# Kernel optimization log

Measured on AMD Instinct MI355X. Metric: run time of the kernel, lower is better.

The kernel has to match this reference:

```python
import jax, jax.numpy as jnp
import numpy as np

B, C, L = 8, 256, 4096
OC = C // 2  # out_channels default
EPS = 1e-5


def setup_inputs() -> dict:
    key = jax.random.key(0)
    ks = jax.random.split(key, 12)
    s_in = 1.0 / np.sqrt(C)   # conv1d default init scale (kaiming-uniform-ish)
    s_oc = 1.0 / np.sqrt(OC)
    return {
        "x": jax.random.normal(ks[0], (B, C, L), dtype=jnp.float32),
        "g_w": jax.random.uniform(ks[1], (OC, C), jnp.float32, -s_in, s_in),
        "g_b": jax.random.uniform(ks[2], (OC,), jnp.float32, -s_in, s_in),
        # theta/phi weights: nn.init.normal_(w, 0.02) -> mean 0.02, std 1
        "theta_w": 0.02 + jax.random.normal(ks[3], (OC, C), dtype=jnp.float32),
        "theta_b": jax.random.uniform(ks[4], (OC,), jnp.float32, -s_in, s_in),
        "phi_w": 0.02 + jax.random.normal(ks[5], (OC, C), dtype=jnp.float32),
        "phi_b": jax.random.uniform(ks[6], (OC,), jnp.float32, -s_in, s_in),
        "W_w": jax.random.uniform(ks[7], (C, OC), jnp.float32, -s_oc, s_oc),
        "W_b": jax.random.uniform(ks[8], (C,), jnp.float32, -s_oc, s_oc),
        # BN affine: init to zero in the original; use small random for a meaningful test
        "gamma": 0.1 * jax.random.normal(ks[9], (C,), dtype=jnp.float32),
        "beta": 0.1 * jax.random.normal(ks[10], (C,), dtype=jnp.float32),
    }


def reference(x, g_w, g_b, theta_w, theta_b, phi_w, phi_b, W_w, W_b, gamma, beta):
    # x: (b, c, l). 1x1 conv == per-position linear map over channels.
    g_x = jnp.einsum('oc,bcl->bol', g_w, x) + g_b[None, :, None]        # (b, oc, l)
    theta_x = jnp.einsum('oc,bcl->bol', theta_w, x) + theta_b[None, :, None]
    phi_x = jnp.einsum('oc,bcl->bol', phi_w, x) + phi_b[None, :, None]
    # f = theta^T phi : (b, l, l) quadratic score matrix (no softmax)
    f = jnp.einsum('bok,bom->bkm', theta_x, phi_x)
    N = f.shape[-1]
    # y = (f @ g^T) / N, returned in (b, oc, l) layout
    y = jnp.einsum('bkm,bom->bok', f, g_x) / N
    W_y = jnp.einsum('co,bol->bcl', W_w, y) + W_b[None, :, None]        # (b, c, l)
    # BatchNorm1d (training mode: batch statistics over (b, l), biased var)
    mean = jnp.mean(W_y, axis=(0, 2), keepdims=True)
    var = jnp.mean((W_y - mean) ** 2, axis=(0, 2), keepdims=True)
    W_y = (W_y - mean) * jax.lax.rsqrt(var + EPS)
    W_y = gamma[None, :, None] * W_y + beta[None, :, None]
    return W_y + x  # residual
```

## Files before the change

kernel.cpp:

```cpp
#include <hip/hip_runtime.h>
#include <hip/hip_bf16.h>

#define B_ 8
#define C_ 256
#define OC_ 128
#define L_ 4096
#define EPS_ 1e-5f
#define SPLITK 8

typedef unsigned short u16;
typedef __attribute__((ext_vector_type(4))) unsigned short u16x4;
typedef __attribute__((ext_vector_type(4))) float f32x4;
typedef __attribute__((ext_vector_type(8))) short bf16x8;

__device__ inline u16 f2bf(float f) {
  union { __hip_bfloat16 h; u16 u; } v;
  v.h = __float2bfloat16(f);
  return v.u;
}
__device__ inline float bf2f(u16 u) {
  union { float f; unsigned u; } v;
  v.u = ((unsigned)u) << 16;
  return v.f;
}

__device__ inline void gload_lds16(const void* g, void* lds) {
  __builtin_amdgcn_global_load_lds(
      (const __attribute__((address_space(1))) unsigned int*)g,
      (__attribute__((address_space(3))) unsigned int*)lds, 16, 0, 0);
}

__global__ __launch_bounds__(256) void k_cvt(const float* __restrict__ x,
                                             u16* __restrict__ Xb,
                                             u16* __restrict__ XbT,
                                             float* __restrict__ spartial) {
  __shared__ u16 T[64][73];
  __shared__ float P[64][17];
  const int b = blockIdx.z, c0 = blockIdx.y * 64, l0 = blockIdx.x * 64;
  const int tid = threadIdx.x;
#pragma unroll
  for (int it = 0; it < 4; ++it) {
    int idx = it * 256 + tid;
    int row = idx >> 4;
    int col = (idx & 15) << 2;
    size_t gi = ((size_t)(b * C_ + c0 + row)) * L_ + l0 + col;
    float4 v = *(const float4*)(x + gi);
    u16 u0 = f2bf(v.x), u1 = f2bf(v.y), u2 = f2bf(v.z), u3 = f2bf(v.w);
    u16x4 u = {u0, u1, u2, u3};
    *(u16x4*)(Xb + gi) = u;
    T[row][col] = u0; T[row][col + 1] = u1; T[row][col + 2] = u2; T[row][col + 3] = u3;
    P[row][idx & 15] = v.x + v.y + v.z + v.w;
  }
  __syncthreads();
  if (tid < 64) {
    float acc = 0.f;
#pragma unroll
    for (int j = 0; j < 16; j++) acc += P[tid][j];
    spartial[(size_t)blockIdx.x * (B_ * C_) + b * C_ + c0 + tid] = acc;
  }
#pragma unroll
  for (int it = 0; it < 4; ++it) {
    int idx = it * 256 + tid;
    int lrow = idx >> 4;
    int ccol = (idx & 15) << 2;
    u16x4 u = {T[ccol][lrow], T[ccol + 1][lrow], T[ccol + 2][lrow], T[ccol + 3][lrow]};
    *(u16x4*)(XbT + ((size_t)b * L_ + l0 + lrow) * C_ + c0 + ccol) = u;
  }
}

__global__ __launch_bounds__(256) void k_xxt(const u16* __restrict__ Xb,
                                             float* __restrict__ Spart) {
  const int b = blockIdx.z, split = blockIdx.y;
  const int ti = blockIdx.x >> 2, tj = blockIdx.x & 3;
  __shared__ u16 lds[2][2][64 * 64];
  const int tid = threadIdx.x, lane = tid & 63;
  const int wid = tid >> 6, wr = wid >> 1, wc = wid & 1;
  const u16* Arows = Xb + ((size_t)b * C_ + ti * 64) * L_;
  const u16* Brows = Xb + ((size_t)b * C_ + tj * 64) * L_;
  const int k0 = split * (L_ / SPLITK);
  f32x4 acc[2][2] = {};

  auto STAGE = [&](int buf, int kt) {
#pragma unroll
    for (int ch = 0; ch < 2; ch++) {
      int d = ch * 4096 + tid * 16;
      int row = d >> 7;
      int kb = (d & 127) ^ ((row & 7) << 4);
      gload_lds16(Arows + (size_t)row * L_ + k0 + kt + (kb >> 1), (char*)lds[buf][0] + d);
      gload_lds16(Brows + (size_t)row * L_ + k0 + kt + (kb >> 1), (char*)lds[buf][1] + d);
    }
  };

  STAGE(0, 0);
  asm volatile("s_waitcnt vmcnt(0)" ::: "memory");
  __syncthreads();
  int cur = 0;
  for (int kt = 0; kt < L_ / SPLITK; kt += 64) {
    if (kt + 64 < L_ / SPLITK) STAGE(cur ^ 1, kt + 64);
#pragma unroll
    for (int kk = 0; kk < 2; kk++) {
      bf16x8 af[2], bfr[2];
#pragma unroll
      for (int m = 0; m < 2; m++) {
        int row = wr * 32 + m * 16 + (lane & 15);
        int kb = ((kk << 6) + ((lane >> 4) << 4)) ^ ((row & 7) << 4);
        af[m] = *(const bf16x8*)((const char*)lds[cur][0] + row * 128 + kb);
      }
#pragma unroll
      for (int n = 0; n < 2; n++) {
        int row = wc * 32 + n * 16 + (lane & 15);
        int kb = ((kk << 6) + ((lane >> 4) << 4)) ^ ((row & 7) << 4);
        bfr[n] = *(const bf16x8*)((const char*)lds[cur][1] + row * 128 + kb);
      }
#pragma unroll
      for (int m = 0; m < 2; m++)
#pragma unroll
        for (int n = 0; n < 2; n++)
          acc[m][n] = __builtin_amdgcn_mfma_f32_16x16x32_bf16(af[m], bfr[n], acc[m][n], 0, 0, 0);
    }
    asm volatile("s_waitcnt vmcnt(0)" ::: "memory");
    __syncthreads();
    cur ^= 1;
  }
  float* Sp = Spart + ((size_t)split * B_ + b) * C_ * C_;
#pragma unroll
  for (int m = 0; m < 2; m++)
#pragma unroll
    for (int n = 0; n < 2; n++) {
      int r0 = ti * 64 + wr * 32 + m * 16 + ((lane >> 4) << 2);
      int c0 = tj * 64 + wc * 32 + n * 16 + (lane & 15);
#pragma unroll
      for (int r = 0; r < 4; r++)
        Sp[(size_t)(r0 + r) * C_ + c0] = acc[m][n][r];
    }
}

__global__ __launch_bounds__(256) void k_sreduce(const float* __restrict__ Spart,
                                                 const float* __restrict__ spartial,
                                                 const float* __restrict__ g_w,
                                                 float* __restrict__ S,
                                                 u16* __restrict__ Sb,
                                                 float* __restrict__ s,
                                                 float* __restrict__ gwT) {
  const int bid = blockIdx.x, tid = threadIdx.x;
  if (bid < (B_ * C_ * C_) / 256) {
    size_t idx = (size_t)bid * 256 + tid;
    float acc = 0.f;
    for (int sp = 0; sp < SPLITK; sp++) acc += Spart[(size_t)sp * B_ * C_ * C_ + idx];
    S[idx] = acc;
    Sb[idx] = f2bf(acc);
  } else if (bid < (B_ * C_ * C_) / 256 + (B_ * C_) / 256) {
    int idx2 = (bid - (B_ * C_ * C_) / 256) * 256 + tid;
    float acc = 0.f;
#pragma unroll 8
    for (int i = 0; i < 64; i++) acc += spartial[(size_t)i * (B_ * C_) + idx2];
    s[idx2] = acc;
  } else {
    int t = bid - ((B_ * C_ * C_) / 256 + (B_ * C_) / 256);
    int o = t * 8 + (tid & 7);
    int cbase = (tid >> 3) * 8;
#pragma unroll
    for (int k = 0; k < 8; k++) {
      int c = cbase + k;
      gwT[c * OC_ + o] = g_w[o * C_ + c];
    }
  }
}

__global__ __launch_bounds__(256) void k_mid1(const float* __restrict__ S,
                                              const float* __restrict__ s,
                                              const float* __restrict__ phi_w,
                                              const float* __restrict__ phi_b,
                                              const float* __restrict__ gwT,
                                              const float* __restrict__ g_b,
                                              float* __restrict__ MT) {
  const int b = blockIdx.x >> 5, ot = blockIdx.x & 31;
  const int tid = threadIdx.x;
  __shared__ float pw[4][257], t2[4][257], sl[256], ps_s[4], pb_s[4], redw[4][4];
  sl[tid] = s[b * C_ + tid];
#pragma unroll
  for (int r = 0; r < 4; r++) pw[r][tid] = phi_w[(ot * 4 + r) * C_ + tid];
  if (tid < 4) pb_s[tid] = phi_b[ot * 4 + tid];
  __syncthreads();
  float acc4[4] = {};
  const float* Sbr = S + (size_t)b * C_ * C_;
#pragma unroll 4
  for (int cp = 0; cp < C_; cp++) {
    float sv = Sbr[(size_t)cp * C_ + tid];
#pragma unroll
    for (int r = 0; r < 4; r++) acc4[r] += pw[r][cp] * sv;
  }
  const int lane = tid & 63, w = tid >> 6;
#pragma unroll
  for (int r = 0; r < 4; r++) {
    float v = pw[r][tid] * sl[tid];
#pragma unroll
    for (int off = 1; off < 64; off <<= 1) v += __shfl_xor(v, off, 64);
    if (lane == 0) redw[w][r] = v;
  }
#pragma unroll
  for (int r = 0; r < 4; r++) t2[r][tid] = acc4[r] + pb_s[r] * sl[tid];
  __syncthreads();
  if (tid < 4) ps_s[tid] = redw[0][tid] + redw[1][tid] + redw[2][tid] + redw[3][tid];
  __syncthreads();
  const int o = tid & 127, half = tid >> 7;
  float m0 = 0.f, m1 = 0.f;
#pragma unroll 4
  for (int c = 0; c < C_; c++) {
    float gv = gwT[c * OC_ + o];
    m0 += t2[half * 2][c] * gv;
    m1 += t2[half * 2 + 1][c] * gv;
  }
  float gb = g_b[o];
  int r0 = half * 2;
  MT[((size_t)b * OC_ + o) * OC_ + ot * 4 + r0]     = m0 + (ps_s[r0] + (float)L_ * pb_s[r0]) * gb;
  MT[((size_t)b * OC_ + o) * OC_ + ot * 4 + r0 + 1] = m1 + (ps_s[r0 + 1] + (float)L_ * pb_s[r0 + 1]) * gb;
}

__global__ __launch_bounds__(256) void k_mid2(const float* __restrict__ MT,
                                              const float* __restrict__ W_w,
                                              const float* __restrict__ theta_w,
                                              const float* __restrict__ theta_b,
                                              const float* __restrict__ W_b,
                                              const float* __restrict__ s,
                                              u16* __restrict__ Qb,
                                              float* __restrict__ qv,
                                              float* __restrict__ qs_g,
                                              float* __restrict__ sum1) {
  const int b = blockIdx.x >> 6, ct = blockIdx.x & 63;
  const int c0 = ct * 4;
  const int tid = threadIdx.x;
  __shared__ float ww[4][OC_], u_s[4][OC_ + 2], s_l[C_], q_s[4], redq[4][4];
  s_l[tid] = s[b * C_ + tid];
#pragma unroll
  for (int i = tid; i < 4 * OC_; i += 256)
    ww[i >> 7][i & 127] = W_w[(c0 + (i >> 7)) * OC_ + (i & 127)];
  __syncthreads();
  const int op = tid & 127, rh = tid >> 7;
  float ua0 = 0.f, ua1 = 0.f;
  const float* MTb = MT + (size_t)b * OC_ * OC_;
#pragma unroll 4
  for (int o = 0; o < OC_; o++) {
    float mv = MTb[(size_t)o * OC_ + op];
    ua0 += ww[rh * 2][o] * mv;
    ua1 += ww[rh * 2 + 1][o] * mv;
  }
  u_s[rh * 2][op] = ua0 * (1.f / (float)L_);
  u_s[rh * 2 + 1][op] = ua1 * (1.f / (float)L_);
  __syncthreads();
  {
    const int r = tid >> 6, lane = tid & 63;
    float v = u_s[r][lane] * theta_b[lane] + u_s[r][lane + 64] * theta_b[lane + 64];
#pragma unroll
    for (int off = 1; off < 64; off <<= 1) v += __shfl_xor(v, off, 64);
    if (lane == 0) {
      float qval = v + W_b[c0 + r];
      q_s[r] = qval;
      qv[b * C_ + c0 + r] = qval;
    }
  }
  float qa[4] = {};
#pragma unroll 2
  for (int o = 0; o < OC_; o++) {
    float tv = theta_w[(size_t)o * C_ + tid];
#pragma unroll
    for (int r = 0; r < 4; r++) qa[r] += u_s[r][o] * tv;
  }
#pragma unroll
  for (int r = 0; r < 4; r++)
    Qb[((size_t)b * C_ + c0 + r) * C_ + tid] = f2bf(qa[r]);
  const int lane = tid & 63, w = tid >> 6;
#pragma unroll
  for (int r = 0; r < 4; r++) {
    float v = qa[r] * s_l[tid];
#pragma unroll
    for (int off = 1; off < 64; off <<= 1) v += __shfl_xor(v, off, 64);
    if (lane == 0) redq[w][r] = v;
  }
  __syncthreads();
  if (tid < 4) {
    float qs = redq[0][tid] + redq[1][tid] + redq[2][tid] + redq[3][tid];
    qs_g[b * C_ + c0 + tid] = qs;
    sum1[b * C_ + c0 + tid] = qs + (float)L_ * q_s[tid];
  }
}

__global__ __launch_bounds__(256) void k_ystat(const u16* __restrict__ Qb,
                                               const u16* __restrict__ Sb,
                                               float* __restrict__ e2part) {
  const int b = blockIdx.z;
  const int chs = blockIdx.y >> 1, ct = blockIdx.y & 1;
  const int ks = blockIdx.x;
  __shared__ u16 lds[2 * 128 * 64];
  __shared__ float e2s[128][2];
  const int tid = threadIdx.x, lane = tid & 63;
  const int wid = tid >> 6, wr = wid >> 1, wc = wid & 1;
  const u16* Abase = Qb + ((size_t)b * C_ + ct * 128) * C_;
  const u16* Bbase = Sb + ((size_t)b * C_ + chs * 128) * C_;
  const int k0 = ks * 64;
  f32x4 acc[4][4] = {};
#pragma unroll
  for (int ch = 0; ch < 4; ch++) {
    int d = ch * 4096 + tid * 16;
    int row = d >> 7;
    int kb = (d & 127) ^ ((row & 7) << 4);
    gload_lds16(Abase + (size_t)row * C_ + k0 + (kb >> 1), (char*)lds + d);
    gload_lds16(Bbase + (size_t)row * C_ + k0 + (kb >> 1), (char*)lds + 16384 + d);
  }
  asm volatile("s_waitcnt vmcnt(0)" ::: "memory");
  __syncthreads();
#pragma unroll
  for (int kk = 0; kk < 2; kk++) {
    bf16x8 af[4], bfr[4];
#pragma unroll
    for (int m = 0; m < 4; m++) {
      int row = wr * 64 + m * 16 + (lane & 15);
      int kb = ((kk << 6) + ((lane >> 4) << 4)) ^ ((row & 7) << 4);
      af[m] = *(const bf16x8*)((const char*)lds + row * 128 + kb);
    }
#pragma unroll
    for (int n = 0; n < 4; n++) {
      int row = wc * 64 + n * 16 + (lane & 15);
      int kb = ((kk << 6) + ((lane >> 4) << 4)) ^ ((row & 7) << 4);
      bfr[n] = *(const bf16x8*)((const char*)lds + 16384 + row * 128 + kb);
    }
#pragma unroll
    for (int m = 0; m < 4; m++)
#pragma unroll
      for (int n = 0; n < 4; n++)
        acc[m][n] = __builtin_amdgcn_mfma_f32_16x16x32_bf16(af[m], bfr[n], acc[m][n], 0, 0, 0);
  }
  float e2a[4][4];
#pragma unroll
  for (int m = 0; m < 4; m++)
#pragma unroll
    for (int r = 0; r < 4; r++) e2a[m][r] = 0.f;
#pragma unroll
  for (int m = 0; m < 4; m++)
#pragma unroll
    for (int n = 0; n < 4; n++) {
      int ch = chs * 128 + wc * 64 + n * 16 + (lane & 15);
#pragma unroll
      for (int r = 0; r < 4; r++) {
        int c_loc = wr * 64 + m * 16 + ((lane >> 4) << 2) + r;
        float q2 = bf2f(Qb[((size_t)b * C_ + ct * 128 + c_loc) * C_ + ch]);
        e2a[m][r] += acc[m][n][r] * q2;
      }
    }
#pragma unroll
  for (int m = 0; m < 4; m++)
#pragma unroll
    for (int r = 0; r < 4; r++) {
      float v = e2a[m][r];
      v += __shfl_xor(v, 1, 64);
      v += __shfl_xor(v, 2, 64);
      v += __shfl_xor(v, 4, 64);
      v += __shfl_xor(v, 8, 64);
      if ((lane & 15) == 0) {
        int c_loc = wr * 64 + m * 16 + ((lane >> 4) << 2) + r;
        e2s[c_loc][wc] = v;
      }
    }
  __syncthreads();
  if (tid < 128)
    e2part[(((size_t)chs * 4 + ks) * B_ + b) * C_ + ct * 128 + tid] =
        e2s[tid][0] + e2s[tid][1];
}

__global__ __launch_bounds__(256) void k_fin(const float* __restrict__ sum1,
                                             const float* __restrict__ e2part,
                                             const float* __restrict__ qv,
                                             const float* __restrict__ qs_g,
                                             const float* __restrict__ gamma,
                                             const float* __restrict__ beta,
                                             float* __restrict__ gsc_g,
                                             float* __restrict__ qp_g) {
  const int b = blockIdx.x, c = threadIdx.x;
  float m = 0.f, e = 0.f;
#pragma unroll
  for (int bb = 0; bb < B_; bb++) {
    m += sum1[bb * C_ + c];
    float e2 = 0.f;
#pragma unroll
    for (int sl = 0; sl < 8; sl++) e2 += e2part[((size_t)sl * B_ + bb) * C_ + c];
    float qq = qv[bb * C_ + c], qs = qs_g[bb * C_ + c];
    e += e2 + 2.f * qq * qs + (float)L_ * qq * qq;
  }
  const float inv_n = 1.f / (float)(B_ * L_);
  m *= inv_n;
  e *= inv_n;
  float var = e - m * m;
  float g = gamma[c] * rsqrtf(var + EPS_);
  if (b == 0) gsc_g[c] = g;
  qp_g[b * C_ + c] = g * (qv[b * C_ + c] - m) + beta[c];
}

__global__ __launch_bounds__(256) void k_out(const u16* __restrict__ Qb,
                                             const float* __restrict__ gsc_g,
                                             const float* __restrict__ qp_g,
                                             const u16* __restrict__ XbT,
                                             const u16* __restrict__ Xb,
                                             float* __restrict__ out) {
  const int b = blockIdx.z, ct = blockIdx.y, lt = blockIdx.x;
  __shared__ u16 lds[2][2 * 128 * 64];
  __shared__ float gsc_s[128], qp_s[128];
  const int tid = threadIdx.x, lane = tid & 63;
  const int wid = tid >> 6, wr = wid >> 1, wc = wid & 1;
  if (tid < 128) {
    gsc_s[tid] = gsc_g[ct * 128 + tid];
    qp_s[tid] = qp_g[b * C_ + ct * 128 + tid];
  }
  const u16* Abase = Qb + ((size_t)b * C_ + ct * 128) * C_;
  const u16* Bbase = XbT + ((size_t)b * L_ + lt * 128) * C_;
  f32x4 acc[4][4] = {};
  auto STAGE = [&](int buf, int k0) {
#pragma unroll
    for (int ch = 0; ch < 4; ch++) {
      int d = ch * 4096 + tid * 16;
      int row = d >> 7;
      int kb = (d & 127) ^ ((row & 7) << 4);
      gload_lds16(Abase + (size_t)row * C_ + k0 + (kb >> 1), (char*)lds[buf] + d);
      gload_lds16(Bbase + (size_t)row * C_ + k0 + (kb >> 1), (char*)lds[buf] + 16384 + d);
    }
  };
  STAGE(0, 0);
  asm volatile("s_waitcnt vmcnt(0)" ::: "memory");
  __syncthreads();
  int cur = 0;
  for (int k0 = 0; k0 < C_; k0 += 64) {
    if (k0 + 64 < C_) STAGE(cur ^ 1, k0 + 64);
#pragma unroll
    for (int kk = 0; kk < 2; kk++) {
      bf16x8 af[4], bfr[4];
#pragma unroll
      for (int m = 0; m < 4; m++) {
        int row = wr * 64 + m * 16 + (lane & 15);
        int kb = ((kk << 6) + ((lane >> 4) << 4)) ^ ((row & 7) << 4);
        af[m] = *(const bf16x8*)((const char*)lds[cur] + row * 128 + kb);
      }
#pragma unroll
      for (int n = 0; n < 4; n++) {
        int row = wc * 64 + n * 16 + (lane & 15);
        int kb = ((kk << 6) + ((lane >> 4) << 4)) ^ ((row & 7) << 4);
        bfr[n] = *(const bf16x8*)((const char*)lds[cur] + 16384 + row * 128 + kb);
      }
#pragma unroll
      for (int m = 0; m < 4; m++)
#pragma unroll
        for (int n = 0; n < 4; n++)
          acc[m][n] = __builtin_amdgcn_mfma_f32_16x16x32_bf16(af[m], bfr[n], acc[m][n], 0, 0, 0);
    }
    asm volatile("s_waitcnt vmcnt(0)" ::: "memory");
    __syncthreads();
    cur ^= 1;
  }
#pragma unroll
  for (int m = 0; m < 4; m++)
#pragma unroll
    for (int n = 0; n < 4; n++) {
      int cl = wr * 64 + m * 16 + ((lane >> 4) << 2);
      int c = ct * 128 + cl;
      int l = lt * 128 + wc * 64 + n * 16 + (lane & 15);
#pragma unroll
      for (int r = 0; r < 4; r++) {
        size_t gi = ((size_t)b * C_ + c + r) * L_ + l;
        out[gi] = gsc_s[cl + r] * acc[m][n][r] + bf2f(Xb[gi]) + qp_s[cl + r];
      }
    }
}

extern "C" void kernel_launch(void* const* d_in, const int* in_sizes, int n_in,
                              void* d_out, int out_size, void* d_ws, size_t ws_size,
                              hipStream_t stream) {
  const float* x       = (const float*)d_in[0];
  const float* g_w     = (const float*)d_in[1];
  const float* g_b     = (const float*)d_in[2];
  const float* theta_w = (const float*)d_in[3];
  const float* theta_b = (const float*)d_in[4];
  const float* phi_w   = (const float*)d_in[5];
  const float* phi_b   = (const float*)d_in[6];
  const float* W_w     = (const float*)d_in[7];
  const float* W_b     = (const float*)d_in[8];
  const float* gamma   = (const float*)d_in[9];
  const float* beta    = (const float*)d_in[10];
  float* out = (float*)d_out;

  float* ws = (float*)d_ws;
  size_t off = 0;
  float* Spart    = ws + off; off += (size_t)SPLITK * B_ * C_ * C_;
  float* S        = ws + off; off += (size_t)B_ * C_ * C_;
  float* spartial = ws + off; off += (size_t)B_ * C_ * 64;
  float* s_       = ws + off; off += B_ * C_;
  float* gwT      = ws + off; off += C_ * OC_;
  float* MT       = ws + off; off += (size_t)B_ * OC_ * OC_;
  float* qv       = ws + off; off += B_ * C_;
  float* qs_g     = ws + off; off += B_ * C_;
  float* sum1     = ws + off; off += B_ * C_;
  float* e2part   = ws + off; off += 8 * B_ * C_;
  float* gsc_g    = ws + off; off += C_;
  float* qp_g     = ws + off; off += B_ * C_;
  u16* Sb  = (u16*)(ws + off); off += (size_t)B_ * C_ * C_ / 2;
  u16* Qb  = (u16*)(ws + off); off += (size_t)B_ * C_ * C_ / 2;
  u16* Xb  = (u16*)(ws + off); off += (size_t)B_ * C_ * L_ / 2;
  u16* XbT = (u16*)(ws + off); off += (size_t)B_ * C_ * L_ / 2;

  k_cvt<<<dim3(L_ / 64, C_ / 64, B_), 256, 0, stream>>>(x, Xb, XbT, spartial);
  k_xxt<<<dim3(16, SPLITK, B_), 256, 0, stream>>>(Xb, Spart);
  k_sreduce<<<(B_ * C_ * C_) / 256 + (B_ * C_) / 256 + 16, 256, 0, stream>>>(
      Spart, spartial, g_w, S, Sb, s_, gwT);
  k_mid1<<<B_ * 32, 256, 0, stream>>>(S, s_, phi_w, phi_b, gwT, g_b, MT);
  k_mid2<<<B_ * 64, 256, 0, stream>>>(MT, W_w, theta_w, theta_b, W_b, s_,
                                      Qb, qv, qs_g, sum1);
  k_ystat<<<dim3(4, 4, B_), 256, 0, stream>>>(Qb, Sb, e2part);
  k_fin<<<B_, 256, 0, stream>>>(sum1, e2part, qv, qs_g, gamma, beta, gsc_g, qp_g);
  k_out<<<dim3(L_ / 128, C_ / 128, B_), 256, 0, stream>>>(
      Qb, gsc_g, qp_g, XbT, Xb, out);
}
```

Before: 126.7 us.

## Fold BN scale and residual identity into Q matrix; drop LDS staging in output GEMM

The BN finalize step moves into a new k_build kernel, which scales each row of Q by the BN gain and adds the identity matrix. The residual x is then produced inside the output GEMM from XbT, so the extra read of Xb in the epilogue goes away. k_out now loads MFMA fragments straight from global memory without LDS double-buffering. The k_cvt transpose tile layout also changes. A side effect is that the residual now goes through bf16 rounding after being summed with the scaled Q, which may cost some accuracy.

```diff
diff --git a/kernel.cpp b/kernel.cpp
--- a/kernel.cpp
+++ b/kernel.cpp
@@ -10,6 +10,7 @@
 
 typedef unsigned short u16;
 typedef __attribute__((ext_vector_type(4))) unsigned short u16x4;
+typedef __attribute__((ext_vector_type(8))) unsigned short u16x8;
 typedef __attribute__((ext_vector_type(4))) float f32x4;
 typedef __attribute__((ext_vector_type(8))) short bf16x8;
 
@@ -34,7 +35,7 @@
                                              u16* __restrict__ Xb,
                                              u16* __restrict__ XbT,
                                              float* __restrict__ spartial) {
-  __shared__ u16 T[64][73];
+  __shared__ u16 T[64 * 65];
   __shared__ float P[64][17];
   const int b = blockIdx.z, c0 = blockIdx.y * 64, l0 = blockIdx.x * 64;
   const int tid = threadIdx.x;
@@ -48,7 +49,10 @@
     u16 u0 = f2bf(v.x), u1 = f2bf(v.y), u2 = f2bf(v.z), u3 = f2bf(v.w);
     u16x4 u = {u0, u1, u2, u3};
     *(u16x4*)(Xb + gi) = u;
-    T[row][col] = u0; T[row][col + 1] = u1; T[row][col + 2] = u2; T[row][col + 3] = u3;
+    T[(col + 0) * 65 + row] = u0;
+    T[(col + 1) * 65 + row] = u1;
+    T[(col + 2) * 65 + row] = u2;
+    T[(col + 3) * 65 + row] = u3;
     P[row][idx & 15] = v.x + v.y + v.z + v.w;
   }
   __syncthreads();
@@ -63,7 +67,8 @@
     int idx = it * 256 + tid;
     int lrow = idx >> 4;
     int ccol = (idx & 15) << 2;
-    u16x4 u = {T[ccol][lrow], T[ccol + 1][lrow], T[ccol + 2][lrow], T[ccol + 3][lrow]};
+    u16x4 u = {T[lrow * 65 + ccol], T[lrow * 65 + ccol + 1],
+               T[lrow * 65 + ccol + 2], T[lrow * 65 + ccol + 3]};
     *(u16x4*)(XbT + ((size_t)b * L_ + l0 + lrow) * C_ + c0 + ccol) = u;
   }
 }
@@ -367,104 +372,105 @@
         e2s[tid][0] + e2s[tid][1];
 }
 
-__global__ __launch_bounds__(256) void k_fin(const float* __restrict__ sum1,
-                                             const float* __restrict__ e2part,
-                                             const float* __restrict__ qv,
-                                             const float* __restrict__ qs_g,
-                                             const float* __restrict__ gamma,
-                                             const float* __restrict__ beta,
-                                             float* __restrict__ gsc_g,
-                                             float* __restrict__ qp_g) {
-  const int b = blockIdx.x, c = threadIdx.x;
-  float m = 0.f, e = 0.f;
-#pragma unroll
-  for (int bb = 0; bb < B_; bb++) {
-    m += sum1[bb * C_ + c];
-    float e2 = 0.f;
-#pragma unroll
-    for (int sl = 0; sl < 8; sl++) e2 += e2part[((size_t)sl * B_ + bb) * C_ + c];
-    float qq = qv[bb * C_ + c], qs = qs_g[bb * C_ + c];
-    e += e2 + 2.f * qq * qs + (float)L_ * qq * qq;
-  }
-  const float inv_n = 1.f / (float)(B_ * L_);
-  m *= inv_n;
-  e *= inv_n;
-  float var = e - m * m;
-  float g = gamma[c] * rsqrtf(var + EPS_);
-  if (b == 0) gsc_g[c] = g;
-  qp_g[b * C_ + c] = g * (qv[b * C_ + c] - m) + beta[c];
-}
-
-__global__ __launch_bounds__(256) void k_out(const u16* __restrict__ Qb,
-                                             const float* __restrict__ gsc_g,
+__global__ __launch_bounds__(256) void k_build(const u16* __restrict__ Qb,
+                                               const float* __restrict__ qv,
+                                               const float* __restrict__ qs_g,
+                                               const float* __restrict__ sum1,
+                                               const float* __restrict__ e2part,
+                                               const float* __restrict__ gamma,
+                                               const float* __restrict__ beta,
+                                               u16* __restrict__ Qs,
+                                               float* __restrict__ qp_g) {
+  const int b = blockIdx.x >> 4, rq = blockIdx.x & 15;
+  const int tid = threadIdx.x;
+  __shared__ float gsc_s[16];
+  if (tid < 16) {
+    int c = rq * 16 + tid;
+    float m = 0.f, e = 0.f;
+#pragma unroll
+    for (int bb = 0; bb < B_; bb++) {
+      m += sum1[bb * C_ + c];
+      float e2 = 0.f;
+#pragma unroll
+      for (int sl = 0; sl < 8; sl++) e2 += e2part[((size_t)sl * B_ + bb) * C_ + c];
+      float qq = qv[bb * C_ + c], qs = qs_g[bb * C_ + c];
+      e += e2 + 2.f * qq * qs + (float)L_ * qq * qq;
+    }
+    const float inv_n = 1.f / (float)(B_ * L_);
+    m *= inv_n;
+    e *= inv_n;
+    float var = e - m * m;
+    float g = gamma[c] * rsqrtf(var + EPS_);
+    gsc_s[tid] = g;
+    qp_g[b * C_ + c] = g * (qv[b * C_ + c] - m) + beta[c];
+  }
+  __syncthreads();
+  const int row = tid >> 4;
+  const int c = rq * 16 + row;
+  const int seg = (tid & 15) * 16;
+  const float g = gsc_s[row];
+  const u16x8* src = (const u16x8*)(Qb + ((size_t)b * C_ + c) * C_ + seg);
+  u16x8 v0 = src[0], v1 = src[1];
+  u16x8 o0, o1;
+#pragma unroll
+  for (int j = 0; j < 8; j++) {
+    float a = g * bf2f(v0[j]);
+    if (seg + j == c) a += 1.f;
+    o0[j] = f2bf(a);
+  }
+#pragma unroll
+  for (int j = 0; j < 8; j++) {
+    float a = g * bf2f(v1[j]);
+    if (seg + 8 + j == c) a += 1.f;
+    o1[j] = f2bf(a);
+  }
+  u16x8* dst = (u16x8*)(Qs + ((size_t)b * C_ + c) * C_ + seg);
+  dst[0] = o0;
+  dst[1] = o1;
+}
+
+__global__ __launch_bounds__(256) void k_out(const u16* __restrict__ Qs,
                                              const float* __restrict__ qp_g,
                                              const u16* __restrict__ XbT,
-                                             const u16* __restrict__ Xb,
                                              float* __restrict__ out) {
   const int b = blockIdx.z, ct = blockIdx.y, lt = blockIdx.x;
-  __shared__ u16 lds[2][2 * 128 * 64];
-  __shared__ float gsc_s[128], qp_s[128];
   const int tid = threadIdx.x, lane = tid & 63;
   const int wid = tid >> 6, wr = wid >> 1, wc = wid & 1;
-  if (tid < 128) {
-    gsc_s[tid] = gsc_g[ct * 128 + tid];
-    qp_s[tid] = qp_g[b * C_ + ct * 128 + tid];
-  }
-  const u16* Abase = Qb + ((size_t)b * C_ + ct * 128) * C_;
-  const u16* Bbase = XbT + ((size_t)b * L_ + lt * 128) * C_;
+  const u16* Ab = Qs + ((size_t)b * C_ + ct * 128) * C_;
+  const u16* Bb = XbT + ((size_t)b * L_ + lt * 128) * C_;
+  const int khalf = (lane >> 4) << 3;
   f32x4 acc[4][4] = {};
-  auto STAGE = [&](int buf, int k0) {
-#pragma unroll
-    for (int ch = 0; ch < 4; ch++) {
-      int d = ch * 4096 + tid * 16;
-      int row = d >> 7;
-      int kb = (d & 127) ^ ((row & 7) << 4);
-      gload_lds16(Abase + (size_t)row * C_ + k0 + (kb >> 1), (char*)lds[buf] + d);
-      gload_lds16(Bbase + (size_t)row * C_ + k0 + (kb >> 1), (char*)lds[buf] + 16384 + d);
-    }
-  };
-  STAGE(0, 0);
-  asm volatile("s_waitcnt vmcnt(0)" ::: "memory");
-  __syncthreads();
-  int cur = 0;
-  for (int k0 = 0; k0 < C_; k0 += 64) {
-    if (k0 + 64 < C_) STAGE(cur ^ 1, k0 + 64);
-#pragma unroll
-    for (int kk = 0; kk < 2; kk++) {
-      bf16x8 af[4], bfr[4];
-#pragma unroll
-      for (int m = 0; m < 4; m++) {
-        int row = wr * 64 + m * 16 + (lane & 15);
-        int kb = ((kk << 6) + ((lane >> 4) << 4)) ^ ((row & 7) << 4);
-        af[m] = *(const bf16x8*)((const char*)lds[cur] + row * 128 + kb);
-      }
-#pragma unroll
-      for (int n = 0; n < 4; n++) {
-        int row = wc * 64 + n * 16 + (lane & 15);
-        int kb = ((kk << 6) + ((lane >> 4) << 4)) ^ ((row & 7) << 4);
-        bfr[n] = *(const bf16x8*)((const char*)lds[cur] + 16384 + row * 128 + kb);
-      }
-#pragma unroll
-      for (int m = 0; m < 4; m++)
-#pragma unroll
-        for (int n = 0; n < 4; n++)
-          acc[m][n] = __builtin_amdgcn_mfma_f32_16x16x32_bf16(af[m], bfr[n], acc[m][n], 0, 0, 0);
-    }
-    asm volatile("s_waitcnt vmcnt(0)" ::: "memory");
-    __syncthreads();
-    cur ^= 1;
-  }
+#pragma unroll 2
+  for (int k0 = 0; k0 < C_; k0 += 32) {
+    bf16x8 af[4], bfr[4];
+#pragma unroll
+    for (int m = 0; m < 4; m++)
+      af[m] = *(const bf16x8*)(Ab + (size_t)(wr * 64 + m * 16 + (lane & 15)) * C_ + k0 + khalf);
+#pragma unroll
+    for (int n = 0; n < 4; n++)
+      bfr[n] = *(const bf16x8*)(Bb + (size_t)(wc * 64 + n * 16 + (lane & 15)) * C_ + k0 + khalf);
+#pragma unroll
+    for (int m = 0; m < 4; m++)
+#pragma unroll
+      for (int n = 0; n < 4; n++)
+        acc[m][n] = __builtin_amdgcn_mfma_f32_16x16x32_bf16(af[m], bfr[n], acc[m][n], 0, 0, 0);
+  }
+  float qpr[4][4];
 #pragma unroll
   for (int m = 0; m < 4; m++)
 #pragma unroll
+    for (int r = 0; r < 4; r++)
+      qpr[m][r] = qp_g[b * C_ + ct * 128 + wr * 64 + m * 16 + ((lane >> 4) << 2) + r];
+#pragma unroll
+  for (int m = 0; m < 4; m++)
+#pragma unroll
     for (int n = 0; n < 4; n++) {
-      int cl = wr * 64 + m * 16 + ((lane >> 4) << 2);
-      int c = ct * 128 + cl;
+      int c = ct * 128 + wr * 64 + m * 16 + ((lane >> 4) << 2);
       int l = lt * 128 + wc * 64 + n * 16 + (lane & 15);
 #pragma unroll
       for (int r = 0; r < 4; r++) {
         size_t gi = ((size_t)b * C_ + c + r) * L_ + l;
-        out[gi] = gsc_s[cl + r] * acc[m][n][r] + bf2f(Xb[gi]) + qp_s[cl + r];
+        out[gi] = acc[m][n][r] + qpr[m][r];
       }
     }
 }
@@ -497,10 +503,10 @@
   float* qs_g     = ws + off; off += B_ * C_;
   float* sum1     = ws + off; off += B_ * C_;
   float* e2part   = ws + off; off += 8 * B_ * C_;
-  float* gsc_g    = ws + off; off += C_;
   float* qp_g     = ws + off; off += B_ * C_;
   u16* Sb  = (u16*)(ws + off); off += (size_t)B_ * C_ * C_ / 2;
   u16* Qb  = (u16*)(ws + off); off += (size_t)B_ * C_ * C_ / 2;
+  u16* Qs  = (u16*)(ws + off); off += (size_t)B_ * C_ * C_ / 2;
   u16* Xb  = (u16*)(ws + off); off += (size_t)B_ * C_ * L_ / 2;
   u16* XbT = (u16*)(ws + off); off += (size_t)B_ * C_ * L_ / 2;
 
@@ -512,7 +518,7 @@
   k_mid2<<<B_ * 64, 256, 0, stream>>>(MT, W_w, theta_w, theta_b, W_b, s_,
                                       Qb, qv, qs_g, sum1);
   k_ystat<<<dim3(4, 4, B_), 256, 0, stream>>>(Qb, Sb, e2part);
-  k_fin<<<B_, 256, 0, stream>>>(sum1, e2part, qv, qs_g, gamma, beta, gsc_g, qp_g);
-  k_out<<<dim3(L_ / 128, C_ / 128, B_), 256, 0, stream>>>(
-      Qb, gsc_g, qp_g, XbT, Xb, out);
-}
+  k_build<<<B_ * 16, 256, 0, stream>>>(Qb, qv, qs_g, sum1, e2part, gamma, beta,
+                                       Qs, qp_g);
+  k_out<<<dim3(L_ / 128, C_ / 128, B_), 256, 0, stream>>>(Qs, qp_g, XbT, out);
+}
```

Result: slower. 133.7 us (+5.5%).

## Fold BN scale and residual identity into output GEMM matrix

Applied to the files above, without the earlier changes.

Replaces the finalize kernel with a build kernel that computes BN scale per channel and writes a scaled copy of Q with identity added on the diagonal, so the output GEMM directly produces gamma-scaled y plus the residual x. This removes the per-element read of the bf16 copy of x and the scale multiply in the output epilogue. As a trade-off the residual now comes through the bf16 GEMM instead of an exact add, which can cost accuracy. SPLITK is also lowered from 8 to 4, which changes how the k_xxt partial products are split.

```diff
diff --git a/kernel.cpp b/kernel.cpp
--- a/kernel.cpp
+++ b/kernel.cpp
@@ -6,10 +6,11 @@
 #define OC_ 128
 #define L_ 4096
 #define EPS_ 1e-5f
-#define SPLITK 8
+#define SPLITK 4
 
 typedef unsigned short u16;
 typedef __attribute__((ext_vector_type(4))) unsigned short u16x4;
+typedef __attribute__((ext_vector_type(8))) unsigned short u16x8;
 typedef __attribute__((ext_vector_type(4))) float f32x4;
 typedef __attribute__((ext_vector_type(8))) short bf16x8;
 
@@ -367,50 +368,74 @@
         e2s[tid][0] + e2s[tid][1];
 }
 
-__global__ __launch_bounds__(256) void k_fin(const float* __restrict__ sum1,
-                                             const float* __restrict__ e2part,
-                                             const float* __restrict__ qv,
-                                             const float* __restrict__ qs_g,
-                                             const float* __restrict__ gamma,
-                                             const float* __restrict__ beta,
-                                             float* __restrict__ gsc_g,
-                                             float* __restrict__ qp_g) {
-  const int b = blockIdx.x, c = threadIdx.x;
-  float m = 0.f, e = 0.f;
-#pragma unroll
-  for (int bb = 0; bb < B_; bb++) {
-    m += sum1[bb * C_ + c];
-    float e2 = 0.f;
-#pragma unroll
-    for (int sl = 0; sl < 8; sl++) e2 += e2part[((size_t)sl * B_ + bb) * C_ + c];
-    float qq = qv[bb * C_ + c], qs = qs_g[bb * C_ + c];
-    e += e2 + 2.f * qq * qs + (float)L_ * qq * qq;
-  }
-  const float inv_n = 1.f / (float)(B_ * L_);
-  m *= inv_n;
-  e *= inv_n;
-  float var = e - m * m;
-  float g = gamma[c] * rsqrtf(var + EPS_);
-  if (b == 0) gsc_g[c] = g;
-  qp_g[b * C_ + c] = g * (qv[b * C_ + c] - m) + beta[c];
-}
-
-__global__ __launch_bounds__(256) void k_out(const u16* __restrict__ Qb,
-                                             const float* __restrict__ gsc_g,
+__global__ __launch_bounds__(256) void k_build(const u16* __restrict__ Qb,
+                                               const float* __restrict__ qv,
+                                               const float* __restrict__ qs_g,
+                                               const float* __restrict__ sum1,
+                                               const float* __restrict__ e2part,
+                                               const float* __restrict__ gamma,
+                                               const float* __restrict__ beta,
+                                               u16* __restrict__ Qs,
+                                               float* __restrict__ qp_g) {
+  const int b = blockIdx.x >> 4, rq = blockIdx.x & 15;
+  const int tid = threadIdx.x;
+  __shared__ float gsc_s[16];
+  if (tid < 16) {
+    int c = rq * 16 + tid;
+    float m = 0.f, e = 0.f;
+#pragma unroll
+    for (int bb = 0; bb < B_; bb++) {
+      m += sum1[bb * C_ + c];
+      float e2 = 0.f;
+#pragma unroll
+      for (int sl = 0; sl < 8; sl++) e2 += e2part[((size_t)sl * B_ + bb) * C_ + c];
+      float qq = qv[bb * C_ + c], qs = qs_g[bb * C_ + c];
+      e += e2 + 2.f * qq * qs + (float)L_ * qq * qq;
+    }
+    const float inv_n = 1.f / (float)(B_ * L_);
+    m *= inv_n;
+    e *= inv_n;
+    float var = e - m * m;
+    float g = gamma[c] * rsqrtf(var + EPS_);
+    gsc_s[tid] = g;
+    qp_g[b * C_ + c] = g * (qv[b * C_ + c] - m) + beta[c];
+  }
+  __syncthreads();
+  const int row = tid >> 4;
+  const int c = rq * 16 + row;
+  const int seg = (tid & 15) * 16;
+  const float g = gsc_s[row];
+  const u16x8* src = (const u16x8*)(Qb + ((size_t)b * C_ + c) * C_ + seg);
+  u16x8 v0 = src[0], v1 = src[1];
+  u16x8 o0, o1;
+#pragma unroll
+  for (int j = 0; j < 8; j++) {
+    float a = g * bf2f(v0[j]);
+    if (seg + j == c) a += 1.f;
+    o0[j] = f2bf(a);
+  }
+#pragma unroll
+  for (int j = 0; j < 8; j++) {
+    float a = g * bf2f(v1[j]);
+    if (seg + 8 + j == c) a += 1.f;
+    o1[j] = f2bf(a);
+  }
+  u16x8* dst = (u16x8*)(Qs + ((size_t)b * C_ + c) * C_ + seg);
+  dst[0] = o0;
+  dst[1] = o1;
+}
+
+__global__ __launch_bounds__(256) void k_out(const u16* __restrict__ Qs,
                                              const float* __restrict__ qp_g,
                                              const u16* __restrict__ XbT,
-                                             const u16* __restrict__ Xb,
                                              float* __restrict__ out) {
   const int b = blockIdx.z, ct = blockIdx.y, lt = blockIdx.x;
   __shared__ u16 lds[2][2 * 128 * 64];
-  __shared__ float gsc_s[128], qp_s[128];
+  __shared__ float qp_s[128];
   const int tid = threadIdx.x, lane = tid & 63;
   const int wid = tid >> 6, wr = wid >> 1, wc = wid & 1;
-  if (tid < 128) {
-    gsc_s[tid] = gsc_g[ct * 128 + tid];
-    qp_s[tid] = qp_g[b * C_ + ct * 128 + tid];
-  }
-  const u16* Abase = Qb + ((size_t)b * C_ + ct * 128) * C_;
+  if (tid < 128) qp_s[tid] = qp_g[b * C_ + ct * 128 + tid];
+  const u16* Abase = Qs + ((size_t)b * C_ + ct * 128) * C_;
   const u16* Bbase = XbT + ((size_t)b * L_ + lt * 128) * C_;
   f32x4 acc[4][4] = {};
   auto STAGE = [&](int buf, int k0) {
@@ -464,7 +489,7 @@
 #pragma unroll
       for (int r = 0; r < 4; r++) {
         size_t gi = ((size_t)b * C_ + c + r) * L_ + l;
-        out[gi] = gsc_s[cl + r] * acc[m][n][r] + bf2f(Xb[gi]) + qp_s[cl + r];
+        out[gi] = acc[m][n][r] + qp_s[cl + r];
       }
     }
 }
@@ -497,10 +522,10 @@
   float* qs_g     = ws + off; off += B_ * C_;
   float* sum1     = ws + off; off += B_ * C_;
   float* e2part   = ws + off; off += 8 * B_ * C_;
-  float* gsc_g    = ws + off; off += C_;
   float* qp_g     = ws + off; off += B_ * C_;
   u16* Sb  = (u16*)(ws + off); off += (size_t)B_ * C_ * C_ / 2;
   u16* Qb  = (u16*)(ws + off); off += (size_t)B_ * C_ * C_ / 2;
+  u16* Qs  = (u16*)(ws + off); off += (size_t)B_ * C_ * C_ / 2;
   u16* Xb  = (u16*)(ws + off); off += (size_t)B_ * C_ * L_ / 2;
   u16* XbT = (u16*)(ws + off); off += (size_t)B_ * C_ * L_ / 2;
 
@@ -512,7 +537,7 @@
   k_mid2<<<B_ * 64, 256, 0, stream>>>(MT, W_w, theta_w, theta_b, W_b, s_,
                                       Qb, qv, qs_g, sum1);
   k_ystat<<<dim3(4, 4, B_), 256, 0, stream>>>(Qb, Sb, e2part);
-  k_fin<<<B_, 256, 0, stream>>>(sum1, e2part, qv, qs_g, gamma, beta, gsc_g, qp_g);
-  k_out<<<dim3(L_ / 128, C_ / 128, B_), 256, 0, stream>>>(
-      Qb, gsc_g, qp_g, XbT, Xb, out);
-}
+  k_build<<<B_ * 16, 256, 0, stream>>>(Qb, qv, qs_g, sum1, e2part, gamma, beta,
+                                       Qs, qp_g);
+  k_out<<<dim3(L_ / 128, C_ / 128, B_), 256, 0, stream>>>(Qs, qp_g, XbT, out);
+}
```

Result: faster. 120.3 us (-5.1%).

## Fuse BN finalize into output GEMM and fold residual into scaled A

Applied to the files above, without the earlier changes.

Removes the separate k_fin launch by having each k_out block recompute the BatchNorm scale and shift for its 128 channels. The residual x is folded into the GEMM by scaling Q rows by gamma*rsqrt(var) and adding the identity on the diagonal, so the epilogue no longer reads Xb. The A tile now goes through registers to be transformed before its LDS write instead of a direct global-to-LDS load. SPLITK is also halved for the X·Xᵀ split. Risks: x is now added in bf16 inside the MFMA rather than as an fp32 epilogue add, and each block redundantly recomputes the statistics.

```diff
diff --git a/kernel.cpp b/kernel.cpp
--- a/kernel.cpp
+++ b/kernel.cpp
@@ -6,10 +6,11 @@
 #define OC_ 128
 #define L_ 4096
 #define EPS_ 1e-5f
-#define SPLITK 8
+#define SPLITK 4
 
 typedef unsigned short u16;
 typedef __attribute__((ext_vector_type(4))) unsigned short u16x4;
+typedef __attribute__((ext_vector_type(8))) unsigned short u16x8;
 typedef __attribute__((ext_vector_type(4))) float f32x4;
 typedef __attribute__((ext_vector_type(8))) short bf16x8;
 
@@ -367,68 +368,92 @@
         e2s[tid][0] + e2s[tid][1];
 }
 
-__global__ __launch_bounds__(256) void k_fin(const float* __restrict__ sum1,
-                                             const float* __restrict__ e2part,
+__global__ __launch_bounds__(256) void k_out(const u16* __restrict__ Qb,
                                              const float* __restrict__ qv,
                                              const float* __restrict__ qs_g,
+                                             const float* __restrict__ sum1,
+                                             const float* __restrict__ e2part,
                                              const float* __restrict__ gamma,
                                              const float* __restrict__ beta,
-                                             float* __restrict__ gsc_g,
-                                             float* __restrict__ qp_g) {
-  const int b = blockIdx.x, c = threadIdx.x;
-  float m = 0.f, e = 0.f;
-#pragma unroll
-  for (int bb = 0; bb < B_; bb++) {
-    m += sum1[bb * C_ + c];
-    float e2 = 0.f;
-#pragma unroll
-    for (int sl = 0; sl < 8; sl++) e2 += e2part[((size_t)sl * B_ + bb) * C_ + c];
-    float qq = qv[bb * C_ + c], qs = qs_g[bb * C_ + c];
-    e += e2 + 2.f * qq * qs + (float)L_ * qq * qq;
-  }
-  const float inv_n = 1.f / (float)(B_ * L_);
-  m *= inv_n;
-  e *= inv_n;
-  float var = e - m * m;
-  float g = gamma[c] * rsqrtf(var + EPS_);
-  if (b == 0) gsc_g[c] = g;
-  qp_g[b * C_ + c] = g * (qv[b * C_ + c] - m) + beta[c];
-}
-
-__global__ __launch_bounds__(256) void k_out(const u16* __restrict__ Qb,
-                                             const float* __restrict__ gsc_g,
-                                             const float* __restrict__ qp_g,
                                              const u16* __restrict__ XbT,
-                                             const u16* __restrict__ Xb,
                                              float* __restrict__ out) {
   const int b = blockIdx.z, ct = blockIdx.y, lt = blockIdx.x;
-  __shared__ u16 lds[2][2 * 128 * 64];
+  __shared__ u16 Albs[2][128 * 64];
+  __shared__ u16 Blbs[2][128 * 64];
   __shared__ float gsc_s[128], qp_s[128];
   const int tid = threadIdx.x, lane = tid & 63;
   const int wid = tid >> 6, wr = wid >> 1, wc = wid & 1;
   if (tid < 128) {
-    gsc_s[tid] = gsc_g[ct * 128 + tid];
-    qp_s[tid] = qp_g[b * C_ + ct * 128 + tid];
-  }
-  const u16* Abase = Qb + ((size_t)b * C_ + ct * 128) * C_;
+    int c = ct * 128 + tid;
+    float m_ = 0.f, e_ = 0.f;
+#pragma unroll
+    for (int bb = 0; bb < B_; bb++) {
+      m_ += sum1[bb * C_ + c];
+      float e2 = 0.f;
+#pragma unroll
+      for (int sl = 0; sl < 8; sl++) e2 += e2part[((size_t)sl * B_ + bb) * C_ + c];
+      float qq = qv[bb * C_ + c], qs = qs_g[bb * C_ + c];
+      e_ += e2 + 2.f * qq * qs + (float)L_ * qq * qq;
+    }
+    const float inv_n = 1.f / (float)(B_ * L_);
+    m_ *= inv_n;
+    e_ *= inv_n;
+    float var = e_ - m_ * m_;
+    float g = gamma[c] * rsqrtf(var + EPS_);
+    gsc_s[tid] = g;
+    qp_s[tid] = g * (qv[b * C_ + c] - m_) + beta[c];
+  }
+  __syncthreads();
   const u16* Bbase = XbT + ((size_t)b * L_ + lt * 128) * C_;
   f32x4 acc[4][4] = {};
-  auto STAGE = [&](int buf, int k0) {
+  u16x4 regs[8];
+  const int jr = (tid & 15) * 4;
+  const int rb = tid >> 4;
+  auto LOADA = [&](int k0) {
+#pragma unroll
+    for (int pass = 0; pass < 8; pass++) {
+      int row = pass * 16 + rb;
+      regs[pass] = *(const u16x4*)(Qb + ((size_t)b * C_ + ct * 128 + row) * C_ + k0 + jr);
+    }
+  };
+  auto WRITEA = [&](int buf, int k0) {
+#pragma unroll
+    for (int pass = 0; pass < 8; pass++) {
+      int row = pass * 16 + rb;
+      float g = gsc_s[row];
+      int c = ct * 128 + row;
+      u16x4 h;
+#pragma unroll
+      for (int i = 0; i < 4; i++) {
+        float a = g * bf2f(regs[pass][i]);
+        if (k0 + jr + i == c) a += 1.f;
+        h[i] = f2bf(a);
+      }
+      int byte = (jr * 2) ^ ((row & 7) << 4);
+      *(u16x4*)((char*)Albs[buf] + row * 128 + byte) = h;
+    }
+  };
+  auto STAGEB = [&](int buf, int k0) {
 #pragma unroll
     for (int ch = 0; ch < 4; ch++) {
       int d = ch * 4096 + tid * 16;
       int row = d >> 7;
       int kb = (d & 127) ^ ((row & 7) << 4);
-      gload_lds16(Abase + (size_t)row * C_ + k0 + (kb >> 1), (char*)lds[buf] + d);
-      gload_lds16(Bbase + (size_t)row * C_ + k0 + (kb >> 1), (char*)lds[buf] + 16384 + d);
+      gload_lds16(Bbase + (size_t)row * C_ + k0 + (kb >> 1), (char*)Blbs[buf] + d);
     }
   };
-  STAGE(0, 0);
+  LOADA(0);
+  STAGEB(0, 0);
   asm volatile("s_waitcnt vmcnt(0)" ::: "memory");
+  WRITEA(0, 0);
   __syncthreads();
   int cur = 0;
   for (int k0 = 0; k0 < C_; k0 += 64) {
-    if (k0 + 64 < C_) STAGE(cur ^ 1, k0 + 64);
+    bool hasNext = (k0 + 64 < C_);
+    if (hasNext) {
+      STAGEB(cur ^ 1, k0 + 64);
+      LOADA(k0 + 64);
+    }
 #pragma unroll
     for (int kk = 0; kk < 2; kk++) {
       bf16x8 af[4], bfr[4];
@@ -436,13 +461,13 @@
       for (int m = 0; m < 4; m++) {
         int row = wr * 64 + m * 16 + (lane & 15);
         int kb = ((kk << 6) + ((lane >> 4) << 4)) ^ ((row & 7) << 4);
-        af[m] = *(const bf16x8*)((const char*)lds[cur] + row * 128 + kb);
+        af[m] = *(const bf16x8*)((const char*)Albs[cur] + row * 128 + kb);
       }
 #pragma unroll
       for (int n = 0; n < 4; n++) {
         int row = wc * 64 + n * 16 + (lane & 15);
         int kb = ((kk << 6) + ((lane >> 4) << 4)) ^ ((row & 7) << 4);
-        bfr[n] = *(const bf16x8*)((const char*)lds[cur] + 16384 + row * 128 + kb);
+        bfr[n] = *(const bf16x8*)((const char*)Blbs[cur] + row * 128 + kb);
       }
 #pragma unroll
       for (int m = 0; m < 4; m++)
@@ -450,7 +475,10 @@
         for (int n = 0; n < 4; n++)
           acc[m][n] = __builtin_amdgcn_mfma_f32_16x16x32_bf16(af[m], bfr[n], acc[m][n], 0, 0, 0);
     }
-    asm volatile("s_waitcnt vmcnt(0)" ::: "memory");
+    if (hasNext) {
+      asm volatile("s_waitcnt vmcnt(0)" ::: "memory");
+      WRITEA(cur ^ 1, k0 + 64);
+    }
     __syncthreads();
     cur ^= 1;
   }
@@ -464,7 +492,7 @@
 #pragma unroll
       for (int r = 0; r < 4; r++) {
         size_t gi = ((size_t)b * C_ + c + r) * L_ + l;
-        out[gi] = gsc_s[cl + r] * acc[m][n][r] + bf2f(Xb[gi]) + qp_s[cl + r];
+        out[gi] = acc[m][n][r] + qp_s[cl + r];
       }
     }
 }
@@ -497,8 +525,6 @@
   float* qs_g     = ws + off; off += B_ * C_;
   float* sum1     = ws + off; off += B_ * C_;
   float* e2part   = ws + off; off += 8 * B_ * C_;
-  float* gsc_g    = ws + off; off += C_;
-  float* qp_g     = ws + off; off += B_ * C_;
   u16* Sb  = (u16*)(ws + off); off += (size_t)B_ * C_ * C_ / 2;
   u16* Qb  = (u16*)(ws + off); off += (size_t)B_ * C_ * C_ / 2;
   u16* Xb  = (u16*)(ws + off); off += (size_t)B_ * C_ * L_ / 2;
@@ -512,7 +538,6 @@
   k_mid2<<<B_ * 64, 256, 0, stream>>>(MT, W_w, theta_w, theta_b, W_b, s_,
                                       Qb, qv, qs_g, sum1);
   k_ystat<<<dim3(4, 4, B_), 256, 0, stream>>>(Qb, Sb, e2part);
-  k_fin<<<B_, 256, 0, stream>>>(sum1, e2part, qv, qs_g, gamma, beta, gsc_g, qp_g);
   k_out<<<dim3(L_ / 128, C_ / 128, B_), 256, 0, stream>>>(
-      Qb, gsc_g, qp_g, XbT, Xb, out);
-}
+      Qb, qv, qs_g, sum1, e2part, gamma, beta, XbT, out);
+}
```

Measured after the change: 121.0 us. -4.5%, faster.
